# Performance work log

Measured on AMD Instinct MI355X. Metric: run time of the kernel, lower is better.

## Reference

```python
import jax, jax.numpy as jnp
import numpy as np

N_NODES = 100000
N_EDGES = 1600000
IN_CH, HID_CH, OUT_CH = 128, 64, 64


def setup_inputs() -> dict:
    key = jax.random.key(0)
    k1, k2, k3, k4 = jax.random.split(key, 4)
    x = jax.random.normal(k1, (N_NODES, IN_CH), dtype=jnp.float32)
    edge_index = jax.random.randint(k2, (2, N_EDGES), 0, N_NODES, dtype=jnp.int64)
    # Glorot-style init for GCNConv linear weights; zero bias (PyG default)
    W1 = jax.random.normal(k3, (IN_CH, HID_CH), dtype=jnp.float32) * (1.0 / np.sqrt(IN_CH))
    b1 = jnp.zeros((HID_CH,), dtype=jnp.float32)
    W2 = jax.random.normal(k4, (HID_CH, OUT_CH), dtype=jnp.float32) * (1.0 / np.sqrt(HID_CH))
    b2 = jnp.zeros((OUT_CH,), dtype=jnp.float32)
    return {"x": x, "edge_index": edge_index, "W1": W1, "b1": b1, "W2": W2, "b2": b2}


def gcn_conv(x, row, col, W, b):
    # PyG GCNConv: linear transform, then sym-normalized scatter-add aggregation
    h = x @ W  # [N, out]
    ones = jnp.ones(col.shape, dtype=h.dtype)
    deg = jax.ops.segment_sum(ones, col, num_segments=N_NODES)  # in-degree incl. self-loops
    dinv = jnp.where(deg > 0, jax.lax.rsqrt(deg), 0.0)
    norm = dinv[row] * dinv[col]  # [E+N]
    msg = h[row] * norm[:, None]  # gather + scale, [E+N, out]
    out = jax.ops.segment_sum(msg, col, num_segments=N_NODES)  # scatter-add
    return out + b


def reference(x, edge_index, W1, b1, W2, b2):
    # add self-loops once (same edge set for both layers)
    loops = jnp.arange(N_NODES, dtype=edge_index.dtype)
    row = jnp.concatenate([edge_index[0], loops])
    col = jnp.concatenate([edge_index[1], loops])
    h = jax.nn.relu(gcn_conv(x, row, col, W1, b1))
    return gcn_conv(h, row, col, W2, b2)
```

## Files before the change

kernel.cpp:

```cpp
#include <hip/hip_runtime.h>


#define BKT_SH 7
#define BKT_CAP 6144
#define CHUNK 6144
#define BM 128
#define BK 32

__device__ __forceinline__ unsigned short f2bf(float f) {
    unsigned u = __builtin_bit_cast(unsigned, f);
    u = (u + 0x7FFF + ((u >> 16) & 1)) >> 16;
    return (unsigned short)u;
}
__device__ __forceinline__ float bf2f(unsigned short h) {
    unsigned u = ((unsigned)h) << 16;
    return __builtin_bit_cast(float, u);
}

__global__ __launch_bounds__(256) void k_zero_i(int* __restrict__ p, int n) {
    int i = blockIdx.x * 256 + threadIdx.x;
    if (i < n) p[i] = 0;
}

__global__ __launch_bounds__(256) void k_bhist(const int* __restrict__ col,
                                               int* __restrict__ bhist,
                                               int nb, int E) {
    __shared__ int h[1024];
    for (int i = threadIdx.x; i < 1024; i += 256) h[i] = 0;
    __syncthreads();
    int stride = gridDim.x * 256;
    for (int i = blockIdx.x * 256 + threadIdx.x; i < E; i += stride)
        atomicAdd(&h[col[i] >> BKT_SH], 1);
    __syncthreads();
    for (int i = threadIdx.x; i < nb; i += 256)
        if (h[i]) atomicAdd(&bhist[i], h[i]);
}

__global__ __launch_bounds__(1024) void k_bscan(const int* __restrict__ bhist,
                                                int* __restrict__ bucket_base,
                                                int* __restrict__ cursor,
                                                int nb, int E) {
    __shared__ int s[1024];
    int t = threadIdx.x;
    int v = (t < nb) ? bhist[t] : 0;
    s[t] = v;
    __syncthreads();
#pragma unroll
    for (int d = 1; d < 1024; d <<= 1) {
        int x = (t >= d) ? s[t - d] : 0;
        __syncthreads();
        if (t >= d) s[t] += x;
        __syncthreads();
    }
    if (t < nb) {
        int ex = s[t] - v;
        bucket_base[t] = ex;
        cursor[t] = ex;
    }
    if (t == 0) bucket_base[nb] = E;
}

__global__ __launch_bounds__(256) void k_bin(const int* __restrict__ row,
                                             const int* __restrict__ col,
                                             int* __restrict__ cursor,
                                             unsigned* __restrict__ bentries,
                                             int E) {
    __shared__ unsigned sorted[CHUNK];
    __shared__ unsigned short bof[CHUNK];
    __shared__ int hist[1024];
    __shared__ int ex0[1024];
    __shared__ int cur[1024];
    __shared__ int gbase[1024];
    __shared__ int tsum[256];
    int b = blockIdx.x, t = threadIdx.x;
    int s0 = b * CHUNK;
    int cnt = E - s0; if (cnt > CHUNK) cnt = CHUNK;

    for (int i = t; i < 1024; i += 256) hist[i] = 0;
    __syncthreads();
    for (int i = t; i < cnt; i += 256)
        atomicAdd(&hist[col[s0 + i] >> BKT_SH], 1);
    __syncthreads();
    {
        int b0 = hist[4 * t], b1 = hist[4 * t + 1], b2 = hist[4 * t + 2], b3 = hist[4 * t + 3];
        int tot = b0 + b1 + b2 + b3;
        tsum[t] = tot;
        __syncthreads();
#pragma unroll
        for (int d = 1; d < 256; d <<= 1) {
            int x = (t >= d) ? tsum[t - d] : 0;
            __syncthreads();
            tsum[t] += (t >= d) ? x : 0;
            __syncthreads();
        }
        int ex = tsum[t] - tot;
        ex0[4 * t] = ex;
        ex0[4 * t + 1] = ex + b0;
        ex0[4 * t + 2] = ex + b0 + b1;
        ex0[4 * t + 3] = ex + b0 + b1 + b2;
        cur[4 * t] = ex0[4 * t];
        cur[4 * t + 1] = ex0[4 * t + 1];
        cur[4 * t + 2] = ex0[4 * t + 2];
        cur[4 * t + 3] = ex0[4 * t + 3];
    }
    __syncthreads();
    for (int i = t; i < 1024; i += 256)
        if (hist[i] > 0) gbase[i] = atomicAdd(&cursor[i], hist[i]);
    for (int i = t; i < cnt; i += 256) {
        int c = col[s0 + i], r = row[s0 + i];
        int bkt = c >> BKT_SH;
        int p = atomicAdd(&cur[bkt], 1);
        sorted[p] = ((unsigned)(c & ((1 << BKT_SH) - 1)) << 17) | (unsigned)r;
        bof[p] = (unsigned short)bkt;
    }
    __syncthreads();
    for (int i = t; i < cnt; i += 256) {
        int bkt = bof[i];
        bentries[gbase[bkt] + (i - ex0[bkt])] = sorted[i];
    }
}

__global__ __launch_bounds__(256) void k_bucket_sort(
    const unsigned* __restrict__ bentries, const int* __restrict__ bucket_base,
    int* __restrict__ offsets, float* __restrict__ dinv,
    int* __restrict__ eros, int N, int E) {
    __shared__ int hist[128];
    __shared__ int incl[128];
    __shared__ int cur[128];
    __shared__ int rows[BKT_CAP];
    int b = blockIdx.x, t = threadIdx.x;
    int base = bucket_base[b];
    int cnt = bucket_base[b + 1] - base;
    if (cnt > BKT_CAP) cnt = BKT_CAP;

    if (t < 128) hist[t] = 0;
    __syncthreads();
    for (int i = t; i < cnt; i += 256)
        atomicAdd(&hist[bentries[base + i] >> 17], 1);
    __syncthreads();
    if (t < 128) incl[t] = hist[t];
    __syncthreads();
#pragma unroll
    for (int d = 1; d < 128; d <<= 1) {
        int x = (t < 128 && t >= d) ? incl[t - d] : 0;
        __syncthreads();
        if (t < 128 && t >= d) incl[t] += x;
        __syncthreads();
    }
    if (t < 128) {
        int ex = incl[t] - hist[t];
        int node = (b << BKT_SH) + t;
        if (node <= N) offsets[node] = base + ex;
        if (node < N) dinv[node] = rsqrtf((float)hist[t] + 1.0f);
        cur[t] = ex;
    }
    __syncthreads();
    for (int i = t; i < cnt; i += 256) {
        unsigned en = bentries[base + i];
        int p = atomicAdd(&cur[en >> 17], 1);
        rows[p] = (int)(en & 0x1FFFF);
    }
    __syncthreads();
    for (int i = t; i < cnt; i += 256) eros[base + i] = rows[i];
}

__global__ __launch_bounds__(256) void k_gemm_tile(
    const float* __restrict__ X, const float* __restrict__ W,
    const float* __restrict__ dinv, unsigned short* __restrict__ outb,
    int N, int K) {
    __shared__ float Xs[BK][BM + 4];
    __shared__ float Ws[BK][64];
    int t = threadIdx.x;
    int bm = blockIdx.x * BM;
    int tm = t >> 4, tn = t & 15;

    float acc[8][4];
#pragma unroll
    for (int i = 0; i < 8; ++i)
#pragma unroll
        for (int j = 0; j < 4; ++j) acc[i][j] = 0.f;

    for (int kb = 0; kb < K; kb += BK) {
#pragma unroll
        for (int it = 0; it < 4; ++it) {
            int r = (t >> 3) + 32 * it;
            int grow = bm + r;
            int k4 = t & 7;
            float4 v = make_float4(0.f, 0.f, 0.f, 0.f);
            if (grow < N) v = *(const float4*)(X + (size_t)grow * K + kb + k4 * 4);
            Xs[k4 * 4 + 0][r] = v.x;
            Xs[k4 * 4 + 1][r] = v.y;
            Xs[k4 * 4 + 2][r] = v.z;
            Xs[k4 * 4 + 3][r] = v.w;
        }
#pragma unroll
        for (int it = 0; it < 2; ++it) {
            int idx = t + 256 * it;
            ((float4*)Ws)[idx] = ((const float4*)(W + (size_t)kb * 64))[idx];
        }
        __syncthreads();
#pragma unroll
        for (int k = 0; k < BK; ++k) {
            float4 xa = *(const float4*)&Xs[k][tm * 8];
            float4 xb = *(const float4*)&Xs[k][tm * 8 + 4];
            float4 w = *(const float4*)&Ws[k][tn * 4];
            float xs[8] = {xa.x, xa.y, xa.z, xa.w, xb.x, xb.y, xb.z, xb.w};
#pragma unroll
            for (int i = 0; i < 8; ++i) {
                acc[i][0] = fmaf(xs[i], w.x, acc[i][0]);
                acc[i][1] = fmaf(xs[i], w.y, acc[i][1]);
                acc[i][2] = fmaf(xs[i], w.z, acc[i][2]);
                acc[i][3] = fmaf(xs[i], w.w, acc[i][3]);
            }
        }
        __syncthreads();
    }
#pragma unroll
    for (int i = 0; i < 8; ++i) {
        int grow = bm + tm * 8 + i;
        if (grow < N) {
            float s = dinv[grow];
            ushort4 v;
            v.x = f2bf(acc[i][0] * s);
            v.y = f2bf(acc[i][1] * s);
            v.z = f2bf(acc[i][2] * s);
            v.w = f2bf(acc[i][3] * s);
            *(ushort4*)(outb + (size_t)grow * 64 + tn * 4) = v;
        }
    }
}

__global__ __launch_bounds__(256) void k_gather(
    const unsigned short* __restrict__ srcb, const int* __restrict__ offsets,
    const int* __restrict__ eros, const float* __restrict__ dinv,
    const float* __restrict__ bias, float* __restrict__ dst, int N, int do_relu) {
    int idx = blockIdx.x * 256 + threadIdx.x;
    int node = idx >> 4;
    if (node >= N) return;
    int l = idx & 15;

    const ushort4* s4 = (const ushort4*)srcb;
    ushort4 sv = s4[(size_t)node * 16 + l];
    float ax = bf2f(sv.x), ay = bf2f(sv.y), az = bf2f(sv.z), aw = bf2f(sv.w);
    int e = offsets[node], eend = offsets[node + 1];
    for (; e + 16 <= eend; e += 16) {
        ushort4 v[16];
#pragma unroll
        for (int j = 0; j < 16; ++j) {
            int r = eros[e + j];
            v[j] = s4[(size_t)r * 16 + l];
        }
#pragma unroll
        for (int j = 0; j < 16; ++j) {
            ax += bf2f(v[j].x);
            ay += bf2f(v[j].y);
            az += bf2f(v[j].z);
            aw += bf2f(v[j].w);
        }
    }
    for (; e + 4 <= eend; e += 4) {
        ushort4 v[4];
#pragma unroll
        for (int j = 0; j < 4; ++j) {
            int r = eros[e + j];
            v[j] = s4[(size_t)r * 16 + l];
        }
#pragma unroll
        for (int j = 0; j < 4; ++j) {
            ax += bf2f(v[j].x);
            ay += bf2f(v[j].y);
            az += bf2f(v[j].z);
            aw += bf2f(v[j].w);
        }
    }
    for (; e < eend; ++e) {
        int r = eros[e];
        ushort4 v = s4[(size_t)r * 16 + l];
        ax += bf2f(v.x); ay += bf2f(v.y); az += bf2f(v.z); aw += bf2f(v.w);
    }
    float sc = dinv[node];
    float4 b = ((const float4*)bias)[l];
    float4 o;
    o.x = ax * sc + b.x;
    o.y = ay * sc + b.y;
    o.z = az * sc + b.z;
    o.w = aw * sc + b.w;
    if (do_relu) {
        o.x = fmaxf(o.x, 0.f);
        o.y = fmaxf(o.y, 0.f);
        o.z = fmaxf(o.z, 0.f);
        o.w = fmaxf(o.w, 0.f);
    }
    ((float4*)dst)[(size_t)node * 16 + l] = o;
}

extern "C" void kernel_launch(void* const* d_in, const int* in_sizes, int n_in,
                              void* d_out, int out_size, void* d_ws, size_t ws_size,
                              hipStream_t stream) {
    const float* x = (const float*)d_in[0];
    const int* ei = (const int*)d_in[1];
    const float* W1 = (const float*)d_in[2];
    const float* b1 = (const float*)d_in[3];
    const float* W2 = (const float*)d_in[4];
    const float* b2 = (const float*)d_in[5];

    int N = in_sizes[0] / 128;
    int E = in_sizes[1] / 2;
    const int* row = ei;
    const int* col = ei + E;
    int nb = (N + (1 << BKT_SH) - 1) >> BKT_SH;

    char* ws = (char*)d_ws;
    int* bhist = (int*)ws;
    int* bucket_base = (int*)(ws + (1 << 14));
    int* cursor = (int*)(ws + (1 << 15));
    int* offsets = (int*)(ws + (1 << 16));
    float* dinv = (float*)(ws + 576 * 1024);
    unsigned* bentries = (unsigned*)(ws + (2 << 20));
    unsigned short* Ab = (unsigned short*)(ws + (2 << 20));
    int* eros = (int*)(ws + (28 << 20));
    float* OUT = (float*)d_out;

    int gemmblk = (N + BM - 1) / BM;
    int binblk = (E + CHUNK - 1) / CHUNK;

    k_zero_i<<<(nb + 255) / 256, 256, 0, stream>>>(bhist, nb);
    k_bhist<<<320, 256, 0, stream>>>(col, bhist, nb, E);
    k_bscan<<<1, 1024, 0, stream>>>(bhist, bucket_base, cursor, nb, E);
    k_bin<<<binblk, 256, 0, stream>>>(row, col, cursor, bentries, E);
    k_bucket_sort<<<nb, 256, 0, stream>>>(bentries, bucket_base, offsets, dinv,
                                          eros, N, E);

    int gblk = (N * 16 + 255) / 256;

    k_gemm_tile<<<gemmblk, 256, 0, stream>>>(x, W1, dinv, Ab, N, 128);
    k_gather<<<gblk, 256, 0, stream>>>(Ab, offsets, eros, dinv, b1, OUT, N, 1);

    k_gemm_tile<<<gemmblk, 256, 0, stream>>>(OUT, W2, dinv, Ab, N, 64);
    k_gather<<<gblk, 256, 0, stream>>>(Ab, offsets, eros, dinv, b2, OUT, N, 0);
}
```

Measured before the change: 275.9 us.

## Use fixed-capacity buckets, bf16 hidden layer, and 8-lane uint4 gather

```diff
diff --git a/kernel.cpp b/kernel.cpp
--- a/kernel.cpp
+++ b/kernel.cpp
@@ -2,7 +2,7 @@
 
 
 #define BKT_SH 7
-#define BKT_CAP 6144
+#define BKT_CAP 4096
 #define CHUNK 6144
 #define BM 128
 #define BK 32
@@ -12,52 +12,16 @@
     u = (u + 0x7FFF + ((u >> 16) & 1)) >> 16;
     return (unsigned short)u;
 }
-__device__ __forceinline__ float bf2f(unsigned short h) {
-    unsigned u = ((unsigned)h) << 16;
-    return __builtin_bit_cast(float, u);
+__device__ __forceinline__ float bflo(unsigned u) {
+    return __builtin_bit_cast(float, u << 16);
+}
+__device__ __forceinline__ float bfhi(unsigned u) {
+    return __builtin_bit_cast(float, u & 0xFFFF0000u);
 }
 
 __global__ __launch_bounds__(256) void k_zero_i(int* __restrict__ p, int n) {
     int i = blockIdx.x * 256 + threadIdx.x;
     if (i < n) p[i] = 0;
-}
-
-__global__ __launch_bounds__(256) void k_bhist(const int* __restrict__ col,
-                                               int* __restrict__ bhist,
-                                               int nb, int E) {
-    __shared__ int h[1024];
-    for (int i = threadIdx.x; i < 1024; i += 256) h[i] = 0;
-    __syncthreads();
-    int stride = gridDim.x * 256;
-    for (int i = blockIdx.x * 256 + threadIdx.x; i < E; i += stride)
-        atomicAdd(&h[col[i] >> BKT_SH], 1);
-    __syncthreads();
-    for (int i = threadIdx.x; i < nb; i += 256)
-        if (h[i]) atomicAdd(&bhist[i], h[i]);
-}
-
-__global__ __launch_bounds__(1024) void k_bscan(const int* __restrict__ bhist,
-                                                int* __restrict__ bucket_base,
-                                                int* __restrict__ cursor,
-                                                int nb, int E) {
-    __shared__ int s[1024];
-    int t = threadIdx.x;
-    int v = (t < nb) ? bhist[t] : 0;
-    s[t] = v;
-    __syncthreads();
-#pragma unroll
-    for (int d = 1; d < 1024; d <<= 1) {
-        int x = (t >= d) ? s[t - d] : 0;
-        __syncthreads();
-        if (t >= d) s[t] += x;
-        __syncthreads();
-    }
-    if (t < nb) {
-        int ex = s[t] - v;
-        bucket_base[t] = ex;
-        cursor[t] = ex;
-    }
-    if (t == 0) bucket_base[nb] = E;
 }
 
 __global__ __launch_bounds__(256) void k_bin(const int* __restrict__ row,
@@ -105,7 +69,7 @@
     }
     __syncthreads();
     for (int i = t; i < 1024; i += 256)
-        if (hist[i] > 0) gbase[i] = atomicAdd(&cursor[i], hist[i]);
+        if (hist[i] > 0) gbase[i] = i * BKT_CAP + atomicAdd(&cursor[i], hist[i]);
     for (int i = t; i < cnt; i += 256) {
         int c = col[s0 + i], r = row[s0 + i];
         int bkt = c >> BKT_SH;
@@ -116,21 +80,22 @@
     __syncthreads();
     for (int i = t; i < cnt; i += 256) {
         int bkt = bof[i];
-        bentries[gbase[bkt] + (i - ex0[bkt])] = sorted[i];
+        int pos = gbase[bkt] + (i - ex0[bkt]);
+        if (pos < (bkt + 1) * BKT_CAP) bentries[pos] = sorted[i];
     }
 }
 
 __global__ __launch_bounds__(256) void k_bucket_sort(
-    const unsigned* __restrict__ bentries, const int* __restrict__ bucket_base,
-    int* __restrict__ offsets, float* __restrict__ dinv,
-    int* __restrict__ eros, int N, int E) {
+    unsigned* __restrict__ bentries, const int* __restrict__ cursor,
+    int* __restrict__ start, int* __restrict__ cntarr,
+    float* __restrict__ dinv, int N) {
     __shared__ int hist[128];
     __shared__ int incl[128];
     __shared__ int cur[128];
     __shared__ int rows[BKT_CAP];
     int b = blockIdx.x, t = threadIdx.x;
-    int base = bucket_base[b];
-    int cnt = bucket_base[b + 1] - base;
+    int base = b * BKT_CAP;
+    int cnt = cursor[b];
     if (cnt > BKT_CAP) cnt = BKT_CAP;
 
     if (t < 128) hist[t] = 0;
@@ -150,8 +115,11 @@
     if (t < 128) {
         int ex = incl[t] - hist[t];
         int node = (b << BKT_SH) + t;
-        if (node <= N) offsets[node] = base + ex;
-        if (node < N) dinv[node] = rsqrtf((float)hist[t] + 1.0f);
+        if (node < N) {
+            start[node] = base + ex;
+            cntarr[node] = hist[t];
+            dinv[node] = rsqrtf((float)hist[t] + 1.0f);
+        }
         cur[t] = ex;
     }
     __syncthreads();
@@ -161,10 +129,10 @@
         rows[p] = (int)(en & 0x1FFFF);
     }
     __syncthreads();
-    for (int i = t; i < cnt; i += 256) eros[base + i] = rows[i];
-}
-
-__global__ __launch_bounds__(256) void k_gemm_tile(
+    for (int i = t; i < cnt; i += 256) bentries[base + i] = (unsigned)rows[i];
+}
+
+__global__ __launch_bounds__(256) void k_gemm_f32in(
     const float* __restrict__ X, const float* __restrict__ W,
     const float* __restrict__ dinv, unsigned short* __restrict__ outb,
     int N, int K) {
@@ -230,68 +198,155 @@
     }
 }
 
+__global__ __launch_bounds__(256) void k_gemm_bf16in(
+    const unsigned short* __restrict__ Xb, const float* __restrict__ W,
+    const float* __restrict__ dinv, unsigned short* __restrict__ outb,
+    int N, int K) {
+    __shared__ float Xs[BK][BM + 4];
+    __shared__ float Ws[BK][64];
+    int t = threadIdx.x;
+    int bm = blockIdx.x * BM;
+    int tm = t >> 4, tn = t & 15;
+
+    float acc[8][4];
+#pragma unroll
+    for (int i = 0; i < 8; ++i)
+#pragma unroll
+        for (int j = 0; j < 4; ++j) acc[i][j] = 0.f;
+
+    for (int kb = 0; kb < K; kb += BK) {
+#pragma unroll
+        for (int it = 0; it < 2; ++it) {
+            int idx = t * 2 + it;
+            int r = idx >> 2;
+            int q = idx & 3;
+            int grow = bm + r;
+            uint4 v = make_uint4(0u, 0u, 0u, 0u);
+            if (grow < N) v = *(const uint4*)(Xb + (size_t)grow * K + kb + q * 8);
+            int k0 = q * 8;
+            Xs[k0 + 0][r] = bflo(v.x); Xs[k0 + 1][r] = bfhi(v.x);
+            Xs[k0 + 2][r] = bflo(v.y); Xs[k0 + 3][r] = bfhi(v.y);
+            Xs[k0 + 4][r] = bflo(v.z); Xs[k0 + 5][r] = bfhi(v.z);
+            Xs[k0 + 6][r] = bflo(v.w); Xs[k0 + 7][r] = bfhi(v.w);
+        }
+#pragma unroll
+        for (int it = 0; it < 2; ++it) {
+            int idx = t + 256 * it;
+            ((float4*)Ws)[idx] = ((const float4*)(W + (size_t)kb * 64))[idx];
+        }
+        __syncthreads();
+#pragma unroll
+        for (int k = 0; k < BK; ++k) {
+            float4 xa = *(const float4*)&Xs[k][tm * 8];
+            float4 xb = *(const float4*)&Xs[k][tm * 8 + 4];
+            float4 w = *(const float4*)&Ws[k][tn * 4];
+            float xs[8] = {xa.x, xa.y, xa.z, xa.w, xb.x, xb.y, xb.z, xb.w};
+#pragma unroll
+            for (int i = 0; i < 8; ++i) {
+                acc[i][0] = fmaf(xs[i], w.x, acc[i][0]);
+                acc[i][1] = fmaf(xs[i], w.y, acc[i][1]);
+                acc[i][2] = fmaf(xs[i], w.z, acc[i][2]);
+                acc[i][3] = fmaf(xs[i], w.w, acc[i][3]);
+            }
+        }
+        __syncthreads();
+    }
+#pragma unroll
+    for (int i = 0; i < 8; ++i) {
+        int grow = bm + tm * 8 + i;
+        if (grow < N) {
+            float s = dinv[grow];
+            ushort4 v;
+            v.x = f2bf(acc[i][0] * s);
+            v.y = f2bf(acc[i][1] * s);
+            v.z = f2bf(acc[i][2] * s);
+            v.w = f2bf(acc[i][3] * s);
+            *(ushort4*)(outb + (size_t)grow * 64 + tn * 4) = v;
+        }
+    }
+}
+
 __global__ __launch_bounds__(256) void k_gather(
-    const unsigned short* __restrict__ srcb, const int* __restrict__ offsets,
-    const int* __restrict__ eros, const float* __restrict__ dinv,
-    const float* __restrict__ bias, float* __restrict__ dst, int N, int do_relu) {
+    const uint4* __restrict__ srcq, const int* __restrict__ eros,
+    const int* __restrict__ start, const int* __restrict__ cntarr,
+    const float* __restrict__ dinv, const float* __restrict__ bias,
+    float* __restrict__ dstf, uint4* __restrict__ dstq, int N, int mode) {
     int idx = blockIdx.x * 256 + threadIdx.x;
-    int node = idx >> 4;
+    int node = idx >> 3;
     if (node >= N) return;
-    int l = idx & 15;
-
-    const ushort4* s4 = (const ushort4*)srcb;
-    ushort4 sv = s4[(size_t)node * 16 + l];
-    float ax = bf2f(sv.x), ay = bf2f(sv.y), az = bf2f(sv.z), aw = bf2f(sv.w);
-    int e = offsets[node], eend = offsets[node + 1];
-    for (; e + 16 <= eend; e += 16) {
-        ushort4 v[16];
-#pragma unroll
-        for (int j = 0; j < 16; ++j) {
+    int l = idx & 7;
+
+    uint4 sv = srcq[(size_t)node * 8 + l];
+    float a0 = bflo(sv.x), a1 = bfhi(sv.x);
+    float a2 = bflo(sv.y), a3 = bfhi(sv.y);
+    float a4 = bflo(sv.z), a5 = bfhi(sv.z);
+    float a6 = bflo(sv.w), a7 = bfhi(sv.w);
+
+    int e = start[node];
+    int eend = e + cntarr[node];
+    for (; e + 8 <= eend; e += 8) {
+        uint4 v[8];
+#pragma unroll
+        for (int j = 0; j < 8; ++j) {
             int r = eros[e + j];
-            v[j] = s4[(size_t)r * 16 + l];
-        }
-#pragma unroll
-        for (int j = 0; j < 16; ++j) {
-            ax += bf2f(v[j].x);
-            ay += bf2f(v[j].y);
-            az += bf2f(v[j].z);
-            aw += bf2f(v[j].w);
+            v[j] = srcq[(size_t)r * 8 + l];
+        }
+#pragma unroll
+        for (int j = 0; j < 8; ++j) {
+            a0 += bflo(v[j].x); a1 += bfhi(v[j].x);
+            a2 += bflo(v[j].y); a3 += bfhi(v[j].y);
+            a4 += bflo(v[j].z); a5 += bfhi(v[j].z);
+            a6 += bflo(v[j].w); a7 += bfhi(v[j].w);
         }
     }
     for (; e + 4 <= eend; e += 4) {
-        ushort4 v[4];
+        uint4 v[4];
 #pragma unroll
         for (int j = 0; j < 4; ++j) {
             int r = eros[e + j];
-            v[j] = s4[(size_t)r * 16 + l];
+            v[j] = srcq[(size_t)r * 8 + l];
         }
 #pragma unroll
         for (int j = 0; j < 4; ++j) {
-            ax += bf2f(v[j].x);
-            ay += bf2f(v[j].y);
-            az += bf2f(v[j].z);
-            aw += bf2f(v[j].w);
+            a0 += bflo(v[j].x); a1 += bfhi(v[j].x);
+            a2 += bflo(v[j].y); a3 += bfhi(v[j].y);
+            a4 += bflo(v[j].z); a5 += bfhi(v[j].z);
+            a6 += bflo(v[j].w); a7 += bfhi(v[j].w);
         }
     }
     for (; e < eend; ++e) {
         int r = eros[e];
-        ushort4 v = s4[(size_t)r * 16 + l];
-        ax += bf2f(v.x); ay += bf2f(v.y); az += bf2f(v.z); aw += bf2f(v.w);
+        uint4 v = srcq[(size_t)r * 8 + l];
+        a0 += bflo(v.x); a1 += bfhi(v.x);
+        a2 += bflo(v.y); a3 += bfhi(v.y);
+        a4 += bflo(v.z); a5 += bfhi(v.z);
+        a6 += bflo(v.w); a7 += bfhi(v.w);
     }
     float sc = dinv[node];
-    float4 b = ((const float4*)bias)[l];
-    float4 o;
-    o.x = ax * sc + b.x;
-    o.y = ay * sc + b.y;
-    o.z = az * sc + b.z;
-    o.w = aw * sc + b.w;
-    if (do_relu) {
-        o.x = fmaxf(o.x, 0.f);
-        o.y = fmaxf(o.y, 0.f);
-        o.z = fmaxf(o.z, 0.f);
-        o.w = fmaxf(o.w, 0.f);
-    }
-    ((float4*)dst)[(size_t)node * 16 + l] = o;
+    const float4* bp = (const float4*)bias;
+    float4 b0 = bp[l * 2], b1 = bp[l * 2 + 1];
+    a0 = a0 * sc + b0.x; a1 = a1 * sc + b0.y;
+    a2 = a2 * sc + b0.z; a3 = a3 * sc + b0.w;
+    a4 = a4 * sc + b1.x; a5 = a5 * sc + b1.y;
+    a6 = a6 * sc + b1.z; a7 = a7 * sc + b1.w;
+    if (mode) {
+        a0 = fmaxf(a0, 0.f); a1 = fmaxf(a1, 0.f);
+        a2 = fmaxf(a2, 0.f); a3 = fmaxf(a3, 0.f);
+        a4 = fmaxf(a4, 0.f); a5 = fmaxf(a5, 0.f);
+        a6 = fmaxf(a6, 0.f); a7 = fmaxf(a7, 0.f);
+        uint4 o;
+        o.x = (unsigned)f2bf(a0) | ((unsigned)f2bf(a1) << 16);
+        o.y = (unsigned)f2bf(a2) | ((unsigned)f2bf(a3) << 16);
+        o.z = (unsigned)f2bf(a4) | ((unsigned)f2bf(a5) << 16);
+        o.w = (unsigned)f2bf(a6) | ((unsigned)f2bf(a7) << 16);
+        dstq[(size_t)node * 8 + l] = o;
+    } else {
+        float4 o0 = make_float4(a0, a1, a2, a3);
+        float4 o1 = make_float4(a4, a5, a6, a7);
+        float4* d = (float4*)(dstf + (size_t)node * 64 + l * 8);
+        d[0] = o0;
+        d[1] = o1;
+    }
 }
 
 extern "C" void kernel_launch(void* const* d_in, const int* in_sizes, int n_in,
@@ -311,31 +366,30 @@
     int nb = (N + (1 << BKT_SH) - 1) >> BKT_SH;
 
     char* ws = (char*)d_ws;
-    int* bhist = (int*)ws;
-    int* bucket_base = (int*)(ws + (1 << 14));
-    int* cursor = (int*)(ws + (1 << 15));
-    int* offsets = (int*)(ws + (1 << 16));
-    float* dinv = (float*)(ws + 576 * 1024);
+    int* cursor = (int*)ws;
+    int* start = (int*)(ws + (1 << 16));
+    int* cntarr = (int*)(ws + (1 << 19));
+    float* dinv = (float*)(ws + 960 * 1024);
     unsigned* bentries = (unsigned*)(ws + (2 << 20));
-    unsigned short* Ab = (unsigned short*)(ws + (2 << 20));
-    int* eros = (int*)(ws + (28 << 20));
-    float* OUT = (float*)d_out;
+    unsigned short* Ab = (unsigned short*)(ws + (15 << 20));
+    unsigned short* Hb = (unsigned short*)d_out;
+    float* OUTF = (float*)d_out;
 
     int gemmblk = (N + BM - 1) / BM;
     int binblk = (E + CHUNK - 1) / CHUNK;
-
-    k_zero_i<<<(nb + 255) / 256, 256, 0, stream>>>(bhist, nb);
-    k_bhist<<<320, 256, 0, stream>>>(col, bhist, nb, E);
-    k_bscan<<<1, 1024, 0, stream>>>(bhist, bucket_base, cursor, nb, E);
+    int gblk = (N * 8 + 255) / 256;
+
+    k_zero_i<<<(nb + 255) / 256, 256, 0, stream>>>(cursor, nb);
     k_bin<<<binblk, 256, 0, stream>>>(row, col, cursor, bentries, E);
-    k_bucket_sort<<<nb, 256, 0, stream>>>(bentries, bucket_base, offsets, dinv,
-                                          eros, N, E);
-
-    int gblk = (N * 16 + 255) / 256;
-
-    k_gemm_tile<<<gemmblk, 256, 0, stream>>>(x, W1, dinv, Ab, N, 128);
-    k_gather<<<gblk, 256, 0, stream>>>(Ab, offsets, eros, dinv, b1, OUT, N, 1);
-
-    k_gemm_tile<<<gemmblk, 256, 0, stream>>>(OUT, W2, dinv, Ab, N, 64);
-    k_gather<<<gblk, 256, 0, stream>>>(Ab, offsets, eros, dinv, b2, OUT, N, 0);
-}
+    k_bucket_sort<<<nb, 256, 0, stream>>>(bentries, cursor, start, cntarr, dinv, N);
+
+    k_gemm_f32in<<<gemmblk, 256, 0, stream>>>(x, W1, dinv, Ab, N, 128);
+    k_gather<<<gblk, 256, 0, stream>>>((const uint4*)Ab, (const int*)bentries,
+                                       start, cntarr, dinv, b1,
+                                       nullptr, (uint4*)Hb, N, 1);
+
+    k_gemm_bf16in<<<gemmblk, 256, 0, stream>>>(Hb, W2, dinv, Ab, N, 64);
+    k_gather<<<gblk, 256, 0, stream>>>((const uint4*)Ab, (const int*)bentries,
+                                       start, cntarr, dinv, b2,
+                                       OUTF, nullptr, N, 0);
+}
```

Result: faster. 246.0 us (-10.8%).
